# Kernel tuning notes

Hardware: AMD Instinct MI355X
Metric: run time of the kernel (lower is better)

The kernel has to match this reference:

```python
import jax, jax.numpy as jnp
import numpy as np
import math

NUM_ITER = 5
FEAT_STRIDE = 16
NUM_BINS = 5
BIN_DISP = 1.0
GAUSS_SIGMA = 1.0
MASK_INIT_FACTOR = 4.0
MIN_FILTER_REG = 1e-3


def apply_filter(feat, w):
    # feat: (I,S,C,H,W), w: (S,C,fH,fW) -> scores (I,S,H0,W0); grouped conv, one filter per sequence
    I, S, C, H, W = feat.shape
    fH, fW = w.shape[-2:]
    pad = ((fH // 2, fH // 2), (fW // 2, fW // 2))
    out = jax.lax.conv_general_dilated(
        feat.reshape(I, S * C, H, W), w, window_strides=(1, 1), padding=pad,
        feature_group_count=S, dimension_numbers=('NCHW', 'OIHW', 'NCHW'))
    return out.reshape(I, S, out.shape[-2], out.shape[-1])


def distance_map(center, output_sz):
    # center: (N,2) in (row,col) feature coords -> (N,NUM_BINS,H0,W0) soft distance histogram
    bin_centers = jnp.arange(NUM_BINS, dtype=jnp.float32) * BIN_DISP
    k0 = jnp.arange(output_sz[0], dtype=jnp.float32)
    k1 = jnp.arange(output_sz[1], dtype=jnp.float32)
    d0 = k0[None, :, None] - center[:, 0][:, None, None]
    d1 = k1[None, None, :] - center[:, 1][:, None, None]
    dist = jnp.sqrt(d0 * d0 + d1 * d1)  # (N,H0,W0)
    bin_diff = dist[:, None] / BIN_DISP - bin_centers[None, :, None, None]
    first = jax.nn.relu(1.0 - jnp.abs(bin_diff[:, :-1]))
    last = jnp.clip(1.0 + bin_diff[:, -1:], 0.0, 1.0)
    return jnp.concatenate([first, last], axis=1)


def setup_inputs():
    key = jax.random.key(0)
    kw, kf, kxy, kwh = jax.random.split(key, 4)
    I, S, C, H, W = 3, 64, 512, 18, 18
    fH = fW = 4
    weights = 0.01 * jax.random.normal(kw, (S, C, fH, fW), jnp.float32)
    feat = jax.random.normal(kf, (I, S, C, H, W), jnp.float32)
    xy = jax.random.uniform(kxy, (I, S, 2), jnp.float32, 60.0, 180.0)
    wh = jax.random.uniform(kwh, (I, S, 2), jnp.float32, 40.0, 100.0)
    bb = jnp.concatenate([xy, wh], axis=-1)  # (x,y,w,h) in image coords, image size 288
    # learned 1x1-conv parameters, initialized exactly as in __init__
    d = jnp.arange(NUM_BINS, dtype=jnp.float32) * BIN_DISP
    init_gauss = jnp.exp(-0.5 * (d / GAUSS_SIGMA) ** 2)
    label_w = init_gauss - init_gauss.min()
    mask_w = MASK_INIT_FACTOR * jnp.tanh(2.0 - d)  # sigmoid mask_act -> init_bias = 0
    spatial_w = jnp.ones((NUM_BINS,), jnp.float32)
    log_step_length = jnp.zeros((1,), jnp.float32)  # log(1.0)
    filter_reg = 0.01 * jnp.ones((1,), jnp.float32)
    return dict(weights=weights, feat=feat, bb=bb, label_w=label_w, mask_w=mask_w,
                spatial_w=spatial_w, log_step_length=log_step_length, filter_reg=filter_reg)


def reference(weights, feat, bb, label_w, mask_w, spatial_w, log_step_length, filter_reg):
    I, S, C, H, W = feat.shape
    fH, fW = weights.shape[-2:]
    out_sz = (H + (fH + 1) % 2, W + (fW + 1) % 2)
    step = jnp.exp(log_step_length)[0]
    reg = jnp.clip(filter_reg[0] * filter_reg[0], MIN_FILTER_REG ** 2, None)
    offset = (jnp.array([fH, fW], jnp.float32) % 2) / 2.0
    center = ((bb[..., :2] + bb[..., 2:] / 2.0) / FEAT_STRIDE).reshape(-1, 2)[:, ::-1] - offset
    dmap = distance_map(center, out_sz)  # (I*S, B, H0, W0)
    label_map = jnp.einsum('nbhw,b->nhw', dmap, label_w).reshape(I, S, *out_sz)
    target_mask = jax.nn.sigmoid(jnp.einsum('nbhw,b->nhw', dmap, mask_w)).reshape(I, S, *out_sz)
    spatial_weight = jnp.einsum('nbhw,b->nhw', dmap, spatial_w).reshape(I, S, *out_sz)
    sample_weight = math.sqrt(1.0 / I) * spatial_weight
    # transpose of the (linear-in-w) correlation == apply_feat_transpose
    _, filt_vjp = jax.vjp(lambda w: apply_filter(feat, w), weights)
    a_lo = (1.0 - target_mask) / 2.0
    a_hi = (1.0 + target_mask) / 2.0
    for _ in range(NUM_ITER):
        scores = apply_filter(feat, weights)
        scores_act = a_lo * jnp.abs(scores) + a_hi * scores   # LeakyReluPar
        score_mask = a_lo * jnp.sign(scores) + a_hi           # LeakyReluParDeriv
        residuals = sample_weight * (scores_act - label_map)
        residuals_mapped = score_mask * (sample_weight * residuals)
        weights_grad = filt_vjp(residuals_mapped)[0] + reg * weights
        scores_grad = sample_weight * (score_mask * apply_filter(feat, weights_grad))
        alpha_num = jnp.sum(weights_grad.reshape(S, -1) ** 2, axis=1)
        alpha_den = jnp.clip(jnp.sum(scores_grad.reshape(I, S, -1) ** 2, axis=(0, 2)) + reg * alpha_num, 1e-8, None)
        alpha = alpha_num / alpha_den
        weights = weights - step * alpha[:, None, None, None] * weights_grad
    return weights
```

## Files before the change

### kernel.cpp

```cpp
#include <hip/hip_runtime.h>
#include <math.h>

#define I_IMG 3
#define S_SEQ 64
#define C_CH  512
#define H_IN  18
#define W_IN  18
#define HW    324
#define OH 19
#define OW 19
#define NPIX 361
#define FT 16
#define NITER 5
#define RPW 24
#define CVS 32
#define CVPX 108
#define CVQ 27
#define SPL 336
#define BPL 352
#define ASTR 360

typedef unsigned int uint;
typedef unsigned short ushort;
typedef float f32x4 __attribute__((ext_vector_type(4)));
typedef short s16x8 __attribute__((ext_vector_type(8)));
typedef uint u32x4 __attribute__((ext_vector_type(4)));

__device__ inline float blk_reduce(float v, float* tmp) {
  #pragma unroll
  for (int o = 32; o > 0; o >>= 1) v += __shfl_down(v, o, 64);
  int lane = threadIdx.x & 63;
  int w = threadIdx.x >> 6;
  if (lane == 0) tmp[w] = v;
  __syncthreads();
  float r = 0.f;
  if (threadIdx.x == 0) {
    int nw = (blockDim.x + 63) >> 6;
    for (int k = 0; k < nw; ++k) r += tmp[k];
  }
  return r;
}

__device__ inline uint pack_bf2(float lo, float hi) {
  uint ul = __float_as_uint(lo);
  uint uh = __float_as_uint(hi);
  ul = (ul + 0x7fffu + ((ul >> 16) & 1u)) >> 16;
  uh = (uh + 0x7fffu + ((uh >> 16) & 1u)) & 0xffff0000u;
  return ul | uh;
}

__device__ inline ushort bf16r(float f) {
  uint u = __float_as_uint(f);
  return (ushort)((u + 0x7fffu + ((u >> 16) & 1u)) >> 16);
}

__device__ inline uint cvtpk(float a, float b) {
  uint r;
  asm("v_cvt_pk_bf16_f32 %0, %1, %2" : "=v"(r) : "v"(a), "v"(b));
  return r;
}

__device__ inline int chperm(int c) { return (c < 256) ? 2 * c : 2 * (c - 256) + 1; }

__global__ __launch_bounds__(256) void convert_k(
    const float* __restrict__ feat, ushort* __restrict__ featT)
{
  __shared__ uint tile[CVPX * CVS];
  int tid = threadIdx.x;
  int n = blockIdx.x;
  int yz = blockIdx.y;
  int k0 = (yz >> 2) * CVS;
  int kt = yz / 3, pt = yz - kt * 3;
  k0 = kt * CVS;
  int p0 = pt * CVPX;
  const float* fbase = feat + (size_t)n * C_CH * HW + p0;

  for (int idx = tid; idx < CVS * CVQ; idx += 256) {
    int k = idx / CVQ, q = idx - k * CVQ;
    int j = k0 + k;
    const float* src = fbase + (size_t)j * HW + 4 * q;
    float4 lo = *(const float4*)src;
    float4 hi = *(const float4*)(src + 256 * HW);
    uint b = (uint)(4 * q) * CVS + (uint)(k ^ (q & 31));
    tile[b] = pack_bf2(lo.x, hi.x);
    tile[b + CVS] = pack_bf2(lo.y, hi.y);
    tile[b + 2 * CVS] = pack_bf2(lo.z, hi.z);
    tile[b + 3 * CVS] = pack_bf2(lo.w, hi.w);
  }
  __syncthreads();

  uint* dTb = (uint*)featT + ((size_t)n * HW + p0) * (C_CH / 2) + k0;
  for (int idx = tid; idx < CVPX * CVS; idx += 256) {
    int px = idx >> 5, k = idx & 31;
    dTb[(size_t)px * (C_CH / 2) + k] = tile[px * CVS + (k ^ ((px >> 2) & 31))];
  }
}

__global__ void prep_k(const float* __restrict__ bb,
                       const float* __restrict__ label_w,
                       const float* __restrict__ mask_w,
                       const float* __restrict__ spatial_w,
                       const float* __restrict__ lsl,
                       const float* __restrict__ freg,
                       float* __restrict__ sw, float* __restrict__ lm,
                       float* __restrict__ alo, float* __restrict__ ahi,
                       float* __restrict__ scal)
{
  int n = blockIdx.x;
  int p = threadIdx.x;
  if (n == 0 && p == 0) {
    scal[0] = expf(lsl[0]);
    scal[1] = fmaxf(freg[0] * freg[0], 1e-6f);
  }
  if (p >= NPIX) return;
  float bx = bb[n * 4 + 0], by = bb[n * 4 + 1];
  float bw = bb[n * 4 + 2], bh = bb[n * 4 + 3];
  float crow = (by + bh * 0.5f) * (1.f / 16.f);
  float ccol = (bx + bw * 0.5f) * (1.f / 16.f);
  int y = p / OW, x = p - (p / OW) * OW;
  float d0 = (float)y - crow, d1 = (float)x - ccol;
  float dist = sqrtf(d0 * d0 + d1 * d1);
  float bins[5];
  #pragma unroll
  for (int b = 0; b < 4; ++b) bins[b] = fmaxf(1.f - fabsf(dist - (float)b), 0.f);
  bins[4] = fminf(fmaxf(dist - 3.f, 0.f), 1.f);
  float lmv = 0.f, mm = 0.f, sp = 0.f;
  #pragma unroll
  for (int b = 0; b < 5; ++b) {
    lmv += bins[b] * label_w[b];
    mm  += bins[b] * mask_w[b];
    sp  += bins[b] * spatial_w[b];
  }
  float tm = 1.f / (1.f + expf(-mm));
  int idx = n * NPIX + p;
  lm[idx]  = lmv;
  sw[idx]  = 0.57735026918962584f * sp;
  alo[idx] = 0.5f * (1.f - tm);
  ahi[idx] = 0.5f * (1.f + tm);
}

__global__ __launch_bounds__(256) void wT_k(
    const float* __restrict__ w, ushort* __restrict__ wTb)
{
  int s = blockIdx.x;
  const float4* pw = (const float4*)(w + (size_t)s * C_CH * FT);
  ushort* wb = wTb + (size_t)s * 16 * 512;
  for (int g = threadIdx.x; g < C_CH * FT / 4; g += 256) {
    int c = g >> 2, tq = (g & 3) * 4;
    float4 v = pw[g];
    int k = chperm(c);
    wb[(tq + 0) * 512 + k] = bf16r(v.x);
    wb[(tq + 1) * 512 + k] = bf16r(v.y);
    wb[(tq + 2) * 512 + k] = bf16r(v.z);
    wb[(tq + 3) * 512 + k] = bf16r(v.w);
  }
}

__global__ __launch_bounds__(256) void mfma_fwd_k(
    const ushort* __restrict__ featT, const ushort* __restrict__ wTb,
    float* __restrict__ S)
{
  int lane = threadIdx.x & 63;
  int wv = threadIdx.x >> 6;
  int n = blockIdx.x;
  int s = n & 63;
  int mtile = blockIdx.y * 4 + wv;
  if (mtile >= 21) return;
  int mrow = lane & 15;
  int kg = lane >> 4;

  const ushort* wb = wTb + ((size_t)s * 16 + mrow) * 512 + kg * 8;
  s16x8 bfrag[16];
  #pragma unroll
  for (int k0 = 0; k0 < 16; ++k0)
    bfrag[k0] = *(const s16x8*)(wb + k0 * 32);

  int p = mtile * 16 + mrow;
  bool pvalid = p < HW;
  const ushort* fa = featT + ((size_t)n * HW + (pvalid ? p : 0)) * 512 + kg * 8;
  s16x8 zero8 = {0, 0, 0, 0, 0, 0, 0, 0};

  f32x4 acc = {0.f, 0.f, 0.f, 0.f};
  #pragma unroll
  for (int k0 = 0; k0 < 16; ++k0) {
    s16x8 afrag = pvalid ? *(const s16x8*)(fa + k0 * 32) : zero8;
    acc = __builtin_amdgcn_mfma_f32_16x16x32_bf16(afrag, bfrag[k0], acc, 0, 0, 0);
  }

  float* dst = S + ((size_t)n * 16 + mrow) * SPL + mtile * 16 + kg * 4;
  *(float4*)dst = make_float4(acc[0], acc[1], acc[2], acc[3]);
}

__global__ __launch_bounds__(256) void mfma_tr_k(
    const float* __restrict__ feat, const float* __restrict__ r,
    float* __restrict__ wgp)
{
  __shared__ __align__(16) float rp[21 * RPW];
  __shared__ __align__(16) ushort Ald[16 * ASTR];
  int tid = threadIdx.x;
  int i = blockIdx.x >> 1;
  int nh = blockIdx.x & 1;
  int s = blockIdx.y;

  for (int idx = tid; idx < 21 * RPW; idx += 256) rp[idx] = 0.f;
  __syncthreads();
  for (int idx = tid; idx < NPIX; idx += 256) {
    int y = idx / OW, x = idx - y * OW;
    rp[(y + 1) * RPW + (x + 1)] = r[(size_t)(i * S_SEQ + s) * NPIX + idx];
  }
  __syncthreads();

  for (int idx = tid; idx < 16 * BPL; idx += 256) {
    int t = idx / BPL, pp = idx - t * BPL;
    ushort val = 0;
    if (pp < HW) {
      int u = pp / 18, vv = pp - u * 18;
      int dy = t >> 2, dx = t & 3;
      val = bf16r(rp[(u + 3 - dy) * RPW + (vv + 3 - dx)]);
    }
    Ald[t * ASTR + pp] = val;
  }
  __syncthreads();

  int lane = tid & 63, wv = tid >> 6;
  int nsub = lane & 15, kg = lane >> 4;

  const ushort* arow = Ald + nsub * ASTR + kg * 8;
  s16x8 afr[11];
  #pragma unroll
  for (int ks = 0; ks < 11; ++ks)
    afr[ks] = *(const s16x8*)(arow + ks * 32);

  size_t nsbase = ((size_t)i * S_SEQ + s) * C_CH;
  #pragma unroll
  for (int j = 0; j < 4; ++j) {
    int nt = nh * 16 + wv * 4 + j;
    int c = nt * 16 + nsub;
    const float* fb = feat + (nsbase + c) * (size_t)HW + kg * 8;
    f32x4 acc = {0.f, 0.f, 0.f, 0.f};
    #pragma unroll
    for (int ks = 0; ks < 10; ++ks) {
      float4 x = *(const float4*)(fb + ks * 32);
      float4 y = *(const float4*)(fb + ks * 32 + 4);
      u32x4 t = {cvtpk(x.x, x.y), cvtpk(x.z, x.w),
                 cvtpk(y.x, y.y), cvtpk(y.z, y.w)};
      s16x8 bf = __builtin_bit_cast(s16x8, t);
      acc = __builtin_amdgcn_mfma_f32_16x16x32_bf16(afr[ks], bf, acc, 0, 0, 0);
    }
    {
      s16x8 bf = {0, 0, 0, 0, 0, 0, 0, 0};
      if (kg == 0) {
        float4 x = *(const float4*)(fb + 320);
        u32x4 t = {cvtpk(x.x, x.y), cvtpk(x.z, x.w), 0u, 0u};
        bf = __builtin_bit_cast(s16x8, t);
      }
      acc = __builtin_amdgcn_mfma_f32_16x16x32_bf16(afr[10], bf, acc, 0, 0, 0);
    }
    float* dst = wgp + (nsbase + c) * FT + kg * 4;
    *(float4*)dst = make_float4(acc[0], acc[1], acc[2], acc[3]);
  }
}

__device__ inline float s_gather(const float* __restrict__ Sp, int yo, int xo) {
  float sv = 0.f;
  #pragma unroll
  for (int dy = 0; dy < 4; ++dy) {
    int yi = yo + dy - 2;
    if (yi < 0 || yi >= H_IN) continue;
    #pragma unroll
    for (int dx = 0; dx < 4; ++dx) {
      int xi = xo + dx - 2;
      if (xi < 0 || xi >= W_IN) continue;
      sv += Sp[(dy * 4 + dx) * SPL + yi * W_IN + xi];
    }
  }
  return sv;
}

__global__ __launch_bounds__(384) void combine0_k(
    const float* __restrict__ S,
    const float* __restrict__ sw, const float* __restrict__ lm,
    const float* __restrict__ alo, const float* __restrict__ ahi,
    float* __restrict__ scores,
    float* __restrict__ mask, float* __restrict__ rbuf)
{
  int n = blockIdx.x;
  int p = threadIdx.x;
  if (p >= NPIX) return;
  int yo = p / OW, xo = p - yo * OW;
  float sv = s_gather(S + (size_t)n * 16 * SPL, yo, xo);
  int idx = n * NPIX + p;
  scores[idx] = sv;
  float lo = alo[idx], hi = ahi[idx], s_w = sw[idx], l_v = lm[idx];
  float sgn = (sv > 0.f) ? 1.f : ((sv < 0.f) ? -1.f : 0.f);
  float actv = lo * fabsf(sv) + hi * sv;
  float msk = lo * sgn + hi;
  mask[idx] = msk;
  rbuf[idx] = msk * s_w * s_w * (actv - l_v);
}

__global__ __launch_bounds__(1024) void combine_wg_k(
    const float* __restrict__ wgp, const float* __restrict__ wcur,
    const float* __restrict__ scal,
    float* __restrict__ wg, ushort* __restrict__ wgTb,
    float* __restrict__ nump)
{
  __shared__ float rtmp[16];
  int s = blockIdx.x;
  int tid = threadIdx.x;
  float regv = scal[1];
  size_t base = (size_t)s * C_CH * FT;
  size_t istr = (size_t)S_SEQ * C_CH * FT;
  const float4* p0 = (const float4*)(wgp + base);
  const float4* p1 = (const float4*)(wgp + istr + base);
  const float4* p2 = (const float4*)(wgp + 2 * istr + base);
  const float4* pw = (const float4*)(wcur + base);
  float4* pg = (float4*)(wg + base);
  ushort* wb = wgTb + (size_t)s * 16 * 512;
  float sq = 0.f;
  for (int g = tid; g < C_CH * FT / 4; g += 1024) {
    float4 a = p0[g], b = p1[g], c = p2[g], w = pw[g];
    float4 v;
    v.x = a.x + b.x + c.x + regv * w.x;
    v.y = a.y + b.y + c.y + regv * w.y;
    v.z = a.z + b.z + c.z + regv * w.z;
    v.w = a.w + b.w + c.w + regv * w.w;
    pg[g] = v;
    sq += v.x * v.x + v.y * v.y + v.z * v.z + v.w * v.w;
    int ch = g >> 2, tq = (g & 3) * 4;
    int k = chperm(ch);
    wb[(tq + 0) * 512 + k] = bf16r(v.x);
    wb[(tq + 1) * 512 + k] = bf16r(v.y);
    wb[(tq + 2) * 512 + k] = bf16r(v.z);
    wb[(tq + 3) * 512 + k] = bf16r(v.w);
  }
  float tot = blk_reduce(sq, rtmp);
  if (tid == 0) nump[s] = tot;
}

__global__ __launch_bounds__(1024) void update_k(
    float* __restrict__ wcur, const float* __restrict__ wg,
    const float* __restrict__ S,
    const float* __restrict__ sw, const float* __restrict__ lm,
    const float* __restrict__ alo, const float* __restrict__ ahi,
    float* __restrict__ scores, float* __restrict__ mask,
    float* __restrict__ rbuf,
    const float* __restrict__ nump, const float* __restrict__ scal)
{
  __shared__ float rtmp[16];
  __shared__ float s_sa;
  int s = blockIdx.x;
  int tid = threadIdx.x;

  float sgl[2];
  float sq = 0.f;
  #pragma unroll
  for (int k = 0; k < 2; ++k) {
    int g = tid + k * 1024;
    sgl[k] = 0.f;
    if (g < I_IMG * NPIX) {
      int i = g / NPIX, p = g - i * NPIX;
      int n = i * S_SEQ + s;
      int yo = p / OW, xo = p - yo * OW;
      float sv = s_gather(S + (size_t)n * 16 * SPL, yo, xo);
      sgl[k] = sv;
      int idx = n * NPIX + p;
      float sg = sw[idx] * mask[idx] * sv;
      sq += sg * sg;
    }
  }
  float den = blk_reduce(sq, rtmp);
  if (tid == 0) {
    float num = nump[s];
    float regv = scal[1], step = scal[0];
    float d = fmaxf(den + regv * num, 1e-8f);
    s_sa = step * (num / d);
  }
  __syncthreads();
  float sa = s_sa;

  float4* w4 = (float4*)(wcur + (size_t)s * (C_CH * FT));
  const float4* g4 = (const float4*)(wg + (size_t)s * (C_CH * FT));
  for (int idx = tid; idx < C_CH * FT / 4; idx += 1024) {
    float4 w = w4[idx], g = g4[idx];
    w.x -= sa * g.x; w.y -= sa * g.y; w.z -= sa * g.z; w.w -= sa * g.w;
    w4[idx] = w;
  }

  #pragma unroll
  for (int k = 0; k < 2; ++k) {
    int g = tid + k * 1024;
    if (g < I_IMG * NPIX) {
      int i = g / NPIX, p = g - i * NPIX;
      int idx = (i * S_SEQ + s) * NPIX + p;
      float sv = scores[idx] - sa * sgl[k];
      scores[idx] = sv;
      float lo = alo[idx], hi = ahi[idx], s_w = sw[idx], l_v = lm[idx];
      float sgn = (sv > 0.f) ? 1.f : ((sv < 0.f) ? -1.f : 0.f);
      float actv = lo * fabsf(sv) + hi * sv;
      float msk = lo * sgn + hi;
      mask[idx] = msk;
      rbuf[idx] = msk * s_w * s_w * (actv - l_v);
    }
  }
}

extern "C" void kernel_launch(void* const* d_in, const int* in_sizes, int n_in,
                              void* d_out, int out_size, void* d_ws, size_t ws_size,
                              hipStream_t stream)
{
  const float* w_in = (const float*)d_in[0];
  const float* feat = (const float*)d_in[1];
  const float* bb   = (const float*)d_in[2];
  const float* lblw = (const float*)d_in[3];
  const float* mskw = (const float*)d_in[4];
  const float* spw  = (const float*)d_in[5];
  const float* lsl  = (const float*)d_in[6];
  const float* freg = (const float*)d_in[7];

  float* base = (float*)d_ws;
  const int NMAP = I_IMG * S_SEQ * NPIX;
  const int NW   = S_SEQ * C_CH * FT;
  float* sw     = base;
  float* lm     = sw + NMAP;
  float* alo    = lm + NMAP;
  float* ahi    = alo + NMAP;
  float* mask   = ahi + NMAP;
  float* rbuf   = mask + NMAP;
  float* scores = rbuf + NMAP;
  float* wcur   = scores + NMAP;
  float* wg     = wcur + NW;
  float* wgp    = wg + NW;
  float* nump   = wgp + 3 * NW;
  float* scal   = nump + S_SEQ;
  float* Sbuf   = scal + 8;
  ushort* wTb   = (ushort*)(Sbuf + (size_t)I_IMG * S_SEQ * 16 * SPL);
  ushort* featT = wTb + (size_t)S_SEQ * 16 * 512;

  convert_k<<<dim3(I_IMG * S_SEQ, 24), 256, 0, stream>>>(feat, featT);
  prep_k<<<I_IMG * S_SEQ, 384, 0, stream>>>(bb, lblw, mskw, spw, lsl, freg,
                                            sw, lm, alo, ahi, scal);
  hipMemcpyAsync(wcur, w_in, (size_t)NW * sizeof(float),
                 hipMemcpyDeviceToDevice, stream);

  wT_k<<<S_SEQ, 256, 0, stream>>>(wcur, wTb);
  mfma_fwd_k<<<dim3(I_IMG * S_SEQ, 6), 256, 0, stream>>>(featT, wTb, Sbuf);
  combine0_k<<<I_IMG * S_SEQ, 384, 0, stream>>>(
      Sbuf, sw, lm, alo, ahi, scores, mask, rbuf);

  for (int it = 0; it < NITER; ++it) {
    mfma_tr_k<<<dim3(6, S_SEQ), 256, 0, stream>>>(feat, rbuf, wgp);
    combine_wg_k<<<S_SEQ, 1024, 0, stream>>>(wgp, wcur, scal, wg, wTb, nump);
    mfma_fwd_k<<<dim3(I_IMG * S_SEQ, 6), 256, 0, stream>>>(featT, wTb, Sbuf);
    update_k<<<S_SEQ, 1024, 0, stream>>>(
        wcur, wg, Sbuf, sw, lm, alo, ahi, scores, mask, rbuf, nump, scal);
  }
  hipMemcpyAsync(d_out, wcur, (size_t)NW * sizeof(float),
                 hipMemcpyDeviceToDevice, stream);
}
```

Measured before the change: 379.8 us.

## Fuse image reduction and gradient combine into transpose MFMA kernel

The transpose-correlation kernel now loops over all three images inside one block and accumulates in registers. It then adds the regularisation term, writes the gradient and its bf16 transposed copy, and emits per-block partial squared norms. This removes the separate combine kernel, one launch per iteration, and the round trip through a three-way partial-gradient buffer. The channel permutation is dropped so featT and the weight transpose use natural channel order, and update_k now sums eight partial norms. In exchange, each block works through the images serially with extra barriers, and the grid is 8x64 instead of 6x64, which gives less parallelism per block.

```diff
diff --git a/kernel.cpp b/kernel.cpp
--- a/kernel.cpp
+++ b/kernel.cpp
@@ -60,8 +60,6 @@
   return r;
 }
 
-__device__ inline int chperm(int c) { return (c < 256) ? 2 * c : 2 * (c - 256) + 1; }
-
 __global__ __launch_bounds__(256) void convert_k(
     const float* __restrict__ feat, ushort* __restrict__ featT)
 {
@@ -69,18 +67,17 @@
   int tid = threadIdx.x;
   int n = blockIdx.x;
   int yz = blockIdx.y;
-  int k0 = (yz >> 2) * CVS;
   int kt = yz / 3, pt = yz - kt * 3;
-  k0 = kt * CVS;
+  int k0 = kt * CVS;
   int p0 = pt * CVPX;
   const float* fbase = feat + (size_t)n * C_CH * HW + p0;
 
   for (int idx = tid; idx < CVS * CVQ; idx += 256) {
     int k = idx / CVQ, q = idx - k * CVQ;
     int j = k0 + k;
-    const float* src = fbase + (size_t)j * HW + 4 * q;
+    const float* src = fbase + (size_t)(2 * j) * HW + 4 * q;
     float4 lo = *(const float4*)src;
-    float4 hi = *(const float4*)(src + 256 * HW);
+    float4 hi = *(const float4*)(src + HW);
     uint b = (uint)(4 * q) * CVS + (uint)(k ^ (q & 31));
     tile[b] = pack_bf2(lo.x, hi.x);
     tile[b + CVS] = pack_bf2(lo.y, hi.y);
@@ -148,11 +145,10 @@
   for (int g = threadIdx.x; g < C_CH * FT / 4; g += 256) {
     int c = g >> 2, tq = (g & 3) * 4;
     float4 v = pw[g];
-    int k = chperm(c);
-    wb[(tq + 0) * 512 + k] = bf16r(v.x);
-    wb[(tq + 1) * 512 + k] = bf16r(v.y);
-    wb[(tq + 2) * 512 + k] = bf16r(v.z);
-    wb[(tq + 3) * 512 + k] = bf16r(v.w);
+    wb[(tq + 0) * 512 + c] = bf16r(v.x);
+    wb[(tq + 1) * 512 + c] = bf16r(v.y);
+    wb[(tq + 2) * 512 + c] = bf16r(v.z);
+    wb[(tq + 3) * 512 + c] = bf16r(v.w);
   }
 }
 
@@ -193,51 +189,51 @@
 
 __global__ __launch_bounds__(256) void mfma_tr_k(
     const float* __restrict__ feat, const float* __restrict__ r,
-    float* __restrict__ wgp)
+    const float* __restrict__ wcur, const float* __restrict__ scal,
+    float* __restrict__ wg, ushort* __restrict__ wTb,
+    float* __restrict__ numpp)
 {
   __shared__ __align__(16) float rp[21 * RPW];
   __shared__ __align__(16) ushort Ald[16 * ASTR];
+  __shared__ float rtmp[4];
   int tid = threadIdx.x;
-  int i = blockIdx.x >> 1;
-  int nh = blockIdx.x & 1;
+  int cb = blockIdx.x;
   int s = blockIdx.y;
-
-  for (int idx = tid; idx < 21 * RPW; idx += 256) rp[idx] = 0.f;
-  __syncthreads();
-  for (int idx = tid; idx < NPIX; idx += 256) {
-    int y = idx / OW, x = idx - y * OW;
-    rp[(y + 1) * RPW + (x + 1)] = r[(size_t)(i * S_SEQ + s) * NPIX + idx];
-  }
-  __syncthreads();
-
-  for (int idx = tid; idx < 16 * BPL; idx += 256) {
-    int t = idx / BPL, pp = idx - t * BPL;
-    ushort val = 0;
-    if (pp < HW) {
-      int u = pp / 18, vv = pp - u * 18;
-      int dy = t >> 2, dx = t & 3;
-      val = bf16r(rp[(u + 3 - dy) * RPW + (vv + 3 - dx)]);
-    }
-    Ald[t * ASTR + pp] = val;
-  }
-  __syncthreads();
-
   int lane = tid & 63, wv = tid >> 6;
   int nsub = lane & 15, kg = lane >> 4;
-
-  const ushort* arow = Ald + nsub * ASTR + kg * 8;
-  s16x8 afr[11];
-  #pragma unroll
-  for (int ks = 0; ks < 11; ++ks)
-    afr[ks] = *(const s16x8*)(arow + ks * 32);
-
-  size_t nsbase = ((size_t)i * S_SEQ + s) * C_CH;
-  #pragma unroll
-  for (int j = 0; j < 4; ++j) {
-    int nt = nh * 16 + wv * 4 + j;
-    int c = nt * 16 + nsub;
-    const float* fb = feat + (nsbase + c) * (size_t)HW + kg * 8;
-    f32x4 acc = {0.f, 0.f, 0.f, 0.f};
+  int c = (cb * 4 + wv) * 16 + nsub;
+  float regv = scal[1];
+
+  for (int idx = tid; idx < 21 * RPW; idx += 256) rp[idx] = 0.f;
+
+  f32x4 acc = {0.f, 0.f, 0.f, 0.f};
+
+  for (int i = 0; i < I_IMG; ++i) {
+    __syncthreads();
+    for (int idx = tid; idx < NPIX; idx += 256) {
+      int y = idx / OW, x = idx - y * OW;
+      rp[(y + 1) * RPW + (x + 1)] = r[(size_t)(i * S_SEQ + s) * NPIX + idx];
+    }
+    __syncthreads();
+    for (int idx = tid; idx < 16 * BPL; idx += 256) {
+      int t = idx / BPL, pp = idx - t * BPL;
+      ushort val = 0;
+      if (pp < HW) {
+        int u = pp / 18, vv = pp - u * 18;
+        int dy = t >> 2, dx = t & 3;
+        val = bf16r(rp[(u + 3 - dy) * RPW + (vv + 3 - dx)]);
+      }
+      Ald[t * ASTR + pp] = val;
+    }
+    __syncthreads();
+
+    const ushort* arow = Ald + nsub * ASTR + kg * 8;
+    s16x8 afr[11];
+    #pragma unroll
+    for (int ks = 0; ks < 11; ++ks)
+      afr[ks] = *(const s16x8*)(arow + ks * 32);
+
+    const float* fb = feat + ((size_t)(i * S_SEQ + s) * C_CH + c) * HW + kg * 8;
     #pragma unroll
     for (int ks = 0; ks < 10; ++ks) {
       float4 x = *(const float4*)(fb + ks * 32);
@@ -256,9 +252,24 @@
       }
       acc = __builtin_amdgcn_mfma_f32_16x16x32_bf16(afr[10], bf, acc, 0, 0, 0);
     }
-    float* dst = wgp + (nsbase + c) * FT + kg * 4;
-    *(float4*)dst = make_float4(acc[0], acc[1], acc[2], acc[3]);
-  }
+  }
+
+  size_t widx = ((size_t)s * C_CH + c) * FT + kg * 4;
+  float4 wv4 = *(const float4*)(wcur + widx);
+  float4 out;
+  out.x = acc[0] + regv * wv4.x;
+  out.y = acc[1] + regv * wv4.y;
+  out.z = acc[2] + regv * wv4.z;
+  out.w = acc[3] + regv * wv4.w;
+  *(float4*)(wg + widx) = out;
+  ushort* wb = wTb + (size_t)s * 16 * 512;
+  wb[(kg * 4 + 0) * 512 + c] = bf16r(out.x);
+  wb[(kg * 4 + 1) * 512 + c] = bf16r(out.y);
+  wb[(kg * 4 + 2) * 512 + c] = bf16r(out.z);
+  wb[(kg * 4 + 3) * 512 + c] = bf16r(out.w);
+  float sq = out.x * out.x + out.y * out.y + out.z * out.z + out.w * out.w;
+  float tot = blk_reduce(sq, rtmp);
+  if (tid == 0) numpp[s * 8 + cb] = tot;
 }
 
 __device__ inline float s_gather(const float* __restrict__ Sp, int yo, int xo) {
@@ -299,45 +310,6 @@
   rbuf[idx] = msk * s_w * s_w * (actv - l_v);
 }
 
-__global__ __launch_bounds__(1024) void combine_wg_k(
-    const float* __restrict__ wgp, const float* __restrict__ wcur,
-    const float* __restrict__ scal,
-    float* __restrict__ wg, ushort* __restrict__ wgTb,
-    float* __restrict__ nump)
-{
-  __shared__ float rtmp[16];
-  int s = blockIdx.x;
-  int tid = threadIdx.x;
-  float regv = scal[1];
-  size_t base = (size_t)s * C_CH * FT;
-  size_t istr = (size_t)S_SEQ * C_CH * FT;
-  const float4* p0 = (const float4*)(wgp + base);
-  const float4* p1 = (const float4*)(wgp + istr + base);
-  const float4* p2 = (const float4*)(wgp + 2 * istr + base);
-  const float4* pw = (const float4*)(wcur + base);
-  float4* pg = (float4*)(wg + base);
-  ushort* wb = wgTb + (size_t)s * 16 * 512;
-  float sq = 0.f;
-  for (int g = tid; g < C_CH * FT / 4; g += 1024) {
-    float4 a = p0[g], b = p1[g], c = p2[g], w = pw[g];
-    float4 v;
-    v.x = a.x + b.x + c.x + regv * w.x;
-    v.y = a.y + b.y + c.y + regv * w.y;
-    v.z = a.z + b.z + c.z + regv * w.z;
-    v.w = a.w + b.w + c.w + regv * w.w;
-    pg[g] = v;
-    sq += v.x * v.x + v.y * v.y + v.z * v.z + v.w * v.w;
-    int ch = g >> 2, tq = (g & 3) * 4;
-    int k = chperm(ch);
-    wb[(tq + 0) * 512 + k] = bf16r(v.x);
-    wb[(tq + 1) * 512 + k] = bf16r(v.y);
-    wb[(tq + 2) * 512 + k] = bf16r(v.z);
-    wb[(tq + 3) * 512 + k] = bf16r(v.w);
-  }
-  float tot = blk_reduce(sq, rtmp);
-  if (tid == 0) nump[s] = tot;
-}
-
 __global__ __launch_bounds__(1024) void update_k(
     float* __restrict__ wcur, const float* __restrict__ wg,
     const float* __restrict__ S,
@@ -345,7 +317,7 @@
     const float* __restrict__ alo, const float* __restrict__ ahi,
     float* __restrict__ scores, float* __restrict__ mask,
     float* __restrict__ rbuf,
-    const float* __restrict__ nump, const float* __restrict__ scal)
+    const float* __restrict__ numpp, const float* __restrict__ scal)
 {
   __shared__ float rtmp[16];
   __shared__ float s_sa;
@@ -371,7 +343,9 @@
   }
   float den = blk_reduce(sq, rtmp);
   if (tid == 0) {
-    float num = nump[s];
+    float num = 0.f;
+    #pragma unroll
+    for (int k = 0; k < 8; ++k) num += numpp[s * 8 + k];
     float regv = scal[1], step = scal[0];
     float d = fmaxf(den + regv * num, 1e-8f);
     s_sa = step * (num / d);
@@ -430,9 +404,8 @@
   float* scores = rbuf + NMAP;
   float* wcur   = scores + NMAP;
   float* wg     = wcur + NW;
-  float* wgp    = wg + NW;
-  float* nump   = wgp + 3 * NW;
-  float* scal   = nump + S_SEQ;
+  float* numpp  = wg + NW;
+  float* scal   = numpp + S_SEQ * 8;
   float* Sbuf   = scal + 8;
   ushort* wTb   = (ushort*)(Sbuf + (size_t)I_IMG * S_SEQ * 16 * SPL);
   ushort* featT = wTb + (size_t)S_SEQ * 16 * 512;
@@ -449,11 +422,11 @@
       Sbuf, sw, lm, alo, ahi, scores, mask, rbuf);
 
   for (int it = 0; it < NITER; ++it) {
-    mfma_tr_k<<<dim3(6, S_SEQ), 256, 0, stream>>>(feat, rbuf, wgp);
-    combine_wg_k<<<S_SEQ, 1024, 0, stream>>>(wgp, wcur, scal, wg, wTb, nump);
+    mfma_tr_k<<<dim3(8, S_SEQ), 256, 0, stream>>>(
+        feat, rbuf, wcur, scal, wg, wTb, numpp);
     mfma_fwd_k<<<dim3(I_IMG * S_SEQ, 6), 256, 0, stream>>>(featT, wTb, Sbuf);
     update_k<<<S_SEQ, 1024, 0, stream>>>(
-        wcur, wg, Sbuf, sw, lm, alo, ahi, scores, mask, rbuf, nump, scal);
+        wcur, wg, Sbuf, sw, lm, alo, ahi, scores, mask, rbuf, numpp, scal);
   }
   hipMemcpyAsync(d_out, wcur, (size_t)NW * sizeof(float),
                  hipMemcpyDeviceToDevice, stream);
```

After: 373.4 us. Within noise of the previous version (-1.7%).
